# Performance work log

Hardware: AMD Instinct MI355X
Metric: run time of the kernel (lower is better)

Reference implementation:

```python
import jax, jax.numpy as jnp
import numpy as np

EPS = 1e-5

def layer_norm(x, g, b):
    mu = jnp.mean(x, axis=-1, keepdims=True)
    var = jnp.mean((x - mu) ** 2, axis=-1, keepdims=True)
    return (x - mu) * jax.lax.rsqrt(var + EPS) * g + b

def setup_inputs() -> dict:
    key = jax.random.key(0)
    ks = jax.random.split(key, 13)
    B, N, C, H = 2, 2048, 1024, 16
    Dff = 4 * C
    s = lambda k, shape, fan_in: jax.random.normal(k, shape, jnp.float32) * (1.0 / np.sqrt(fan_in))
    return {
        "x": jax.random.normal(ks[0], (B, N, C), jnp.float32),
        "ln1_g": jnp.ones((C,), jnp.float32),
        "ln1_b": jnp.zeros((C,), jnp.float32),
        "qkv_w": s(ks[1], (3 * C, C), C),
        "qkv_b": jnp.zeros((3 * C,), jnp.float32),
        "proj_w": s(ks[2], (C, C), C),
        "proj_b": jnp.zeros((C,), jnp.float32),
        "ln2_g": jnp.ones((C,), jnp.float32),
        "ln2_b": jnp.zeros((C,), jnp.float32),
        "fc1_w": s(ks[3], (Dff, C), C),
        "fc1_b": jnp.zeros((Dff,), jnp.float32),
        "fc2_w": s(ks[4], (C, Dff), Dff),
        "fc2_b": jnp.zeros((C,), jnp.float32),
    }

def reference(x, ln1_g, ln1_b, qkv_w, qkv_b, proj_w, proj_b, ln2_g, ln2_b, fc1_w, fc1_b, fc2_w, fc2_b):
    B, N, C = x.shape
    H = 16
    D = C // H
    # --- attention sub-block (pre-norm) ---
    h = layer_norm(x, ln1_g, ln1_b)
    qkv = h @ qkv_w.T + qkv_b                      # [B,N,3C]
    qkv = qkv.reshape(B, N, 3, H, D).transpose(2, 0, 3, 1, 4)  # [3,B,H,N,D]
    q, k, v = qkv[0], qkv[1], qkv[2]
    attn = jnp.einsum('bhnd,bhmd->bhnm', q, k) * (D ** -0.5)   # [B,H,N,N]
    attn = jax.nn.softmax(attn, axis=-1)
    o = jnp.einsum('bhnm,bhmd->bhnd', attn, v)     # [B,H,N,D]
    o = o.transpose(0, 2, 1, 3).reshape(B, N, C)
    x = x + (o @ proj_w.T + proj_b)
    # --- MLP sub-block (pre-norm) ---
    h = layer_norm(x, ln2_g, ln2_b)
    h = jax.nn.gelu(h @ fc1_w.T + fc1_b, approximate=False)
    x = x + (h @ fc2_w.T + fc2_b)
    return x
```

## Files before the change

kernel.cpp:

```cpp
#include <hip/hip_runtime.h>
#include <hip/hip_bf16.h>
#include <math.h>

typedef __bf16 bf16;
typedef __bf16 bf16x8 __attribute__((ext_vector_type(8)));
typedef __bf16 bf16x4 __attribute__((ext_vector_type(4)));
typedef float  f32x4  __attribute__((ext_vector_type(4)));
typedef float  f32x16 __attribute__((ext_vector_type(16)));
typedef int    i32x4  __attribute__((ext_vector_type(4)));

typedef __attribute__((address_space(1))) void gvoid;
typedef __attribute__((address_space(3))) void lvoid;
#define GLOAD_LDS16(gp, lp) __builtin_amdgcn_global_load_lds((gvoid*)(gp), (lvoid*)(lp), 16, 0, 0)

__global__ __launch_bounds__(256) void prep(
    const float* __restrict__ qkvw, const float* __restrict__ projw,
    const float* __restrict__ fc1w, const float* __restrict__ fc2w,
    bf16* __restrict__ qkvw_h, bf16* __restrict__ projw_h,
    bf16* __restrict__ fc1w_h, bf16* __restrict__ fc2w_h,
    const float* __restrict__ x, const float* __restrict__ g,
    const float* __restrict__ b, bf16* __restrict__ h1) {
  int blk = blockIdx.x;
  if (blk < 12288) {
    const float* in; bf16* out; int base;
    if (blk < 3072)      { in = qkvw; out = qkvw_h; base = blk; }
    else if (blk < 4096) { in = projw; out = projw_h; base = blk - 3072; }
    else if (blk < 8192) { in = fc1w; out = fc1w_h; base = blk - 4096; }
    else                 { in = fc2w; out = fc2w_h; base = blk - 8192; }
    int i = (base * 256 + threadIdx.x) * 4;
    f32x4 v = *(const f32x4*)(in + i);
    bf16x4 o;
    #pragma unroll
    for (int e = 0; e < 4; ++e) o[e] = (bf16)v[e];
    *(bf16x4*)(out + i) = o;
    return;
  }
  int w = threadIdx.x >> 6, l = threadIdx.x & 63;
  size_t row = (size_t)(blk - 12288) * 4 + w;
  const float* xr = x + row * 1024;
  float f[16];
  #pragma unroll
  for (int c = 0; c < 4; ++c) {
    f32x4 v = *(const f32x4*)(xr + c * 256 + l * 4);
    #pragma unroll
    for (int e = 0; e < 4; ++e) f[c * 4 + e] = v[e];
  }
  float s = 0.f, ss = 0.f;
  #pragma unroll
  for (int e = 0; e < 16; ++e) { s += f[e]; ss += f[e] * f[e]; }
  #pragma unroll
  for (int d = 1; d < 64; d <<= 1) { s += __shfl_xor(s, d); ss += __shfl_xor(ss, d); }
  float mean = s * (1.f / 1024.f);
  float var  = ss * (1.f / 1024.f) - mean * mean;
  float rstd = rsqrtf(var + 1e-5f);
  #pragma unroll
  for (int c = 0; c < 4; ++c) {
    f32x4 gv = *(const f32x4*)(g + c * 256 + l * 4);
    f32x4 bv = *(const f32x4*)(b + c * 256 + l * 4);
    bf16x4 ov;
    #pragma unroll
    for (int e = 0; e < 4; ++e)
      ov[e] = (bf16)((f[c * 4 + e] - mean) * rstd * gv[e] + bv[e]);
    *(bf16x4*)(h1 + row * 1024 + c * 256 + l * 4) = ov;
  }
}

__global__ __launch_bounds__(256) void ln_f32(const float* __restrict__ x,
    const float* __restrict__ g, const float* __restrict__ b, bf16* __restrict__ out) {
  int w = threadIdx.x >> 6, l = threadIdx.x & 63;
  size_t row = (size_t)blockIdx.x * 4 + w;
  const float* xr = x + row * 1024;
  float f[16];
  #pragma unroll
  for (int c = 0; c < 4; ++c) {
    f32x4 v = *(const f32x4*)(xr + c * 256 + l * 4);
    #pragma unroll
    for (int e = 0; e < 4; ++e) f[c * 4 + e] = v[e];
  }
  float s = 0.f, ss = 0.f;
  #pragma unroll
  for (int e = 0; e < 16; ++e) { s += f[e]; ss += f[e] * f[e]; }
  #pragma unroll
  for (int d = 1; d < 64; d <<= 1) { s += __shfl_xor(s, d); ss += __shfl_xor(ss, d); }
  float mean = s * (1.f / 1024.f);
  float var  = ss * (1.f / 1024.f) - mean * mean;
  float rstd = rsqrtf(var + 1e-5f);
  #pragma unroll
  for (int c = 0; c < 4; ++c) {
    f32x4 gv = *(const f32x4*)(g + c * 256 + l * 4);
    f32x4 bv = *(const f32x4*)(b + c * 256 + l * 4);
    bf16x4 ov;
    #pragma unroll
    for (int e = 0; e < 4; ++e)
      ov[e] = (bf16)((f[c * 4 + e] - mean) * rstd * gv[e] + bv[e]);
    *(bf16x4*)(out + row * 1024 + c * 256 + l * 4) = ov;
  }
}

#define SWZ(tp) ((tp) ^ ((((tp) >> 9) & 1) << 5))
#define STAGE(buf, op, half, kt_) do { \
    const char* gp_ = (const char*)((op) ? Wp : Ap); \
    int t0_ = (op) ? colBase : rowBase; \
    const int P_ = (op) ? 12 : 13; \
    _Pragma("unroll") for (int s_ = 0; s_ < 2; ++s_) { \
      int b14_ = w * 2048 + s_ * 1024; \
      int tb_ = ((b14_ >> P_) << (P_ + 1)) | ((half) << P_) | (b14_ & ((1 << P_) - 1)); \
      int tq_ = SWZ(tb_ + l * 16); \
      GLOAD_LDS16(gp_ + ((size_t)(t0_ + (tq_ >> 7)) * lda + (size_t)(kt_) * 64) * 2 + (tq_ & 127), \
                  smbase + (buf) * 65536 + (op) * 32768 + tb_); \
    } \
  } while (0)
#define LDA(buf, mi, kk) (*(const bf16x8*)(smbase + (buf) * 65536 + \
    SWZ((wm * 128 + (mi) * 16 + lr) * 128 + (kk) * 64 + lg * 16)))
#define LDB(buf, ni, kk) (*(const bf16x8*)(smbase + (buf) * 65536 + 32768 + \
    SWZ((wn * 64 + (ni) * 16 + lr) * 128 + (kk) * 64 + lg * 16)))
#define RD_A(buf, MI0) { _Pragma("unroll") for (int i_ = 0; i_ < 4; ++i_) \
    _Pragma("unroll") for (int k_ = 0; k_ < 2; ++k_) a[i_][k_] = LDA(buf, (MI0) + i_, k_); }
#define RD_B(buf, NI0) { _Pragma("unroll") for (int j_ = 0; j_ < 2; ++j_) \
    _Pragma("unroll") for (int k_ = 0; k_ < 2; ++k_) bq[j_][k_] = LDB(buf, (NI0) + j_, k_); }
#define MFMA16(MI0, NI0) do { __builtin_amdgcn_s_setprio(1); \
    _Pragma("unroll") for (int i_ = 0; i_ < 4; ++i_) \
    _Pragma("unroll") for (int j_ = 0; j_ < 2; ++j_) \
    _Pragma("unroll") for (int k_ = 0; k_ < 2; ++k_) \
      acc[(MI0) + i_][(NI0) + j_] = __builtin_amdgcn_mfma_f32_16x16x32_bf16( \
          a[i_][k_], bq[j_][k_], acc[(MI0) + i_][(NI0) + j_], 0, 0, 0); \
    __builtin_amdgcn_s_setprio(0); } while (0)
#define BARX() __builtin_amdgcn_s_barrier()
#define LGK0() asm volatile("s_waitcnt lgkmcnt(0)")
#define VM4()  asm volatile("s_waitcnt vmcnt(4)")

template<int ACT, int HASBIAS, typename TO>
__global__ __launch_bounds__(512, 2) void gemm256(const bf16* __restrict__ Ap,
    const bf16* __restrict__ Wp, const float* __restrict__ bias,
    TO* __restrict__ out, int lda, int N, int klen, int nbx, size_t outSlice) {
  __shared__ bf16 smem_[2][2][256 * 64];
  char* smbase = (char*)smem_;
  int tid = threadIdx.x, w = tid >> 6, l = tid & 63, lr = l & 15, lg = l >> 4;
  int wm = w >> 2, wn = w & 3;
  int q = gridDim.x >> 3;
  int wg = ((int)blockIdx.x & 7) * q + ((int)blockIdx.x >> 3);
  int rowBase = (wg / nbx) * 256, colBase = (wg % nbx) * 256;
  Ap += (size_t)blockIdx.y * klen;
  Wp += (size_t)blockIdx.y * klen;
  out += (size_t)blockIdx.y * outSlice;

  f32x4 acc[8][4];
  const f32x4 fz = {0.f, 0.f, 0.f, 0.f};
  #pragma unroll
  for (int i = 0; i < 8; ++i)
    #pragma unroll
    for (int j = 0; j < 4; ++j) acc[i][j] = fz;
  bf16x8 a[4][2], bq[2][2];
  int nkt = klen >> 6;

  STAGE(0, 0, 0, 0); STAGE(0, 1, 0, 0); STAGE(0, 0, 1, 0); STAGE(0, 1, 1, 0);
  STAGE(1, 1, 0, 1); STAGE(1, 0, 1, 1);
  VM4(); BARX();

  for (int t = 0; t < nkt; t += 2) {
    int t1 = t + 1;
    int t2 = t + 2 < nkt ? t + 2 : nkt - 1;
    int t3 = t + 3 < nkt ? t + 3 : nkt - 1;
    RD_A(0, 0); RD_B(0, 0);
    STAGE(1, 0, 0, t1); STAGE(1, 1, 1, t1);
    BARX(); LGK0(); MFMA16(0, 0); BARX();
    RD_A(0, 4);
    BARX(); LGK0(); MFMA16(4, 0); BARX();
    RD_B(0, 2);
    STAGE(0, 1, 0, t2);
    BARX(); LGK0(); MFMA16(4, 2); BARX();
    RD_A(0, 0);
    STAGE(0, 0, 1, t2);
    VM4();
    BARX(); LGK0(); MFMA16(0, 2); BARX();
    RD_A(1, 0); RD_B(1, 0);
    STAGE(0, 0, 0, t2); STAGE(0, 1, 1, t2);
    BARX(); LGK0(); MFMA16(0, 0); BARX();
    RD_A(1, 4);
    BARX(); LGK0(); MFMA16(4, 0); BARX();
    RD_B(1, 2);
    STAGE(1, 1, 0, t3);
    BARX(); LGK0(); MFMA16(4, 2); BARX();
    RD_A(1, 0);
    STAGE(1, 0, 1, t3);
    VM4();
    BARX(); LGK0(); MFMA16(0, 2); BARX();
  }

  #pragma unroll
  for (int ni = 0; ni < 4; ++ni) {
    int col = colBase + wn * 64 + ni * 16 + lr;
    float bv = HASBIAS ? bias[col] : 0.f;
    #pragma unroll
    for (int mi = 0; mi < 8; ++mi) {
      #pragma unroll
      for (int jj = 0; jj < 4; ++jj) {
        int row2 = rowBase + wm * 128 + mi * 16 + lg * 4 + jj;
        float v = acc[mi][ni][jj] + bv;
        if constexpr (ACT == 1) v = 0.5f * v * (1.f + erff(v * 0.70710678118f));
        out[(size_t)row2 * N + col] = (TO)v;
      }
    }
  }
}

__global__ __launch_bounds__(256) void projred_ln(const bf16* __restrict__ part,
    const float* __restrict__ x, const float* __restrict__ pb,
    const float* __restrict__ g, const float* __restrict__ bb,
    float* __restrict__ x1, bf16* __restrict__ h2) {
  int w = threadIdx.x >> 6, l = threadIdx.x & 63;
  size_t row = (size_t)blockIdx.x * 4 + w;
  size_t rb = row * 1024;
  float f[16];
  #pragma unroll
  for (int c = 0; c < 4; ++c) {
    int off = c * 256 + l * 4;
    f32x4 v = *(const f32x4*)(x + rb + off);
    v += *(const f32x4*)(pb + off);
    #pragma unroll
    for (int sl = 0; sl < 4; ++sl) {
      bf16x4 pv = *(const bf16x4*)(part + (size_t)sl * 4194304 + rb + off);
      #pragma unroll
      for (int e = 0; e < 4; ++e) v[e] += (float)pv[e];
    }
    *(f32x4*)(x1 + rb + off) = v;
    #pragma unroll
    for (int e = 0; e < 4; ++e) f[c * 4 + e] = v[e];
  }
  float s = 0.f, ss = 0.f;
  #pragma unroll
  for (int e = 0; e < 16; ++e) { s += f[e]; ss += f[e] * f[e]; }
  #pragma unroll
  for (int d = 1; d < 64; d <<= 1) { s += __shfl_xor(s, d); ss += __shfl_xor(ss, d); }
  float mean = s * (1.f / 1024.f);
  float var  = ss * (1.f / 1024.f) - mean * mean;
  float rstd = rsqrtf(var + 1e-5f);
  #pragma unroll
  for (int c = 0; c < 4; ++c) {
    int off = c * 256 + l * 4;
    f32x4 gv = *(const f32x4*)(g + off);
    f32x4 bv = *(const f32x4*)(bb + off);
    bf16x4 ov;
    #pragma unroll
    for (int e = 0; e < 4; ++e)
      ov[e] = (bf16)((f[c * 4 + e] - mean) * rstd * gv[e] + bv[e]);
    *(bf16x4*)(h2 + rb + off) = ov;
  }
}

__global__ __launch_bounds__(256) void fc2_red(const bf16* __restrict__ part,
    const float* __restrict__ x1, const float* __restrict__ bias,
    float* __restrict__ out) {
  int i = (blockIdx.x * 256 + threadIdx.x) * 4;
  f32x4 s = *(const f32x4*)(x1 + i);
  s += *(const f32x4*)(bias + (i & 1023));
  #pragma unroll
  for (int k = 0; k < 4; ++k) {
    bf16x4 pv = *(const bf16x4*)(part + (size_t)k * 4194304 + i);
    #pragma unroll
    for (int e = 0; e < 4; ++e) s[e] += (float)pv[e];
  }
  *(f32x4*)(out + i) = s;
}

template<int ACT, int HASRES, typename TO>
__global__ __launch_bounds__(256) void gemm_bt(const bf16* __restrict__ A,
    const bf16* __restrict__ W, const float* __restrict__ bias,
    const float* __restrict__ res, TO* __restrict__ out, int M, int N, int K) {
  __shared__ bf16 As[128 * 32];
  __shared__ bf16 Bs[128 * 32];
  int tid = threadIdx.x;
  int w = tid >> 6, l = tid & 63;
  int lr = l & 15, lg = l >> 4;
  int wm = w >> 1, wn = w & 1;
  int rowBase = blockIdx.y * 128;
  int colBase = blockIdx.x * 128;
  f32x4 acc[4][4];
  const f32x4 fz = {0.f, 0.f, 0.f, 0.f};
  #pragma unroll
  for (int i = 0; i < 4; ++i)
    #pragma unroll
    for (int j = 0; j < 4; ++j) acc[i][j] = fz;
  for (int kt = 0; kt < K; kt += 32) {
    __syncthreads();
    #pragma unroll
    for (int j = 0; j < 2; ++j) {
      int u = (w * 2 + j) * 64 + l;
      int r = u >> 2, cb = (u & 3) * 8;
      GLOAD_LDS16(A + (size_t)(rowBase + r) * K + kt + cb, As + (w * 2 + j) * 512);
      GLOAD_LDS16(W + (size_t)(colBase + r) * K + kt + cb, Bs + (w * 2 + j) * 512);
    }
    __syncthreads();
    bf16x8 af[4], bfr[4];
    #pragma unroll
    for (int mi = 0; mi < 4; ++mi)
      af[mi] = *(const bf16x8*)(As + (wm * 64 + mi * 16 + lr) * 32 + lg * 8);
    #pragma unroll
    for (int ni = 0; ni < 4; ++ni)
      bfr[ni] = *(const bf16x8*)(Bs + (wn * 64 + ni * 16 + lr) * 32 + lg * 8);
    #pragma unroll
    for (int mi = 0; mi < 4; ++mi)
      #pragma unroll
      for (int ni = 0; ni < 4; ++ni)
        acc[mi][ni] = __builtin_amdgcn_mfma_f32_16x16x32_bf16(af[mi], bfr[ni], acc[mi][ni], 0, 0, 0);
  }
  #pragma unroll
  for (int ni = 0; ni < 4; ++ni) {
    int col = colBase + wn * 64 + ni * 16 + lr;
    float bv = bias[col];
    #pragma unroll
    for (int mi = 0; mi < 4; ++mi) {
      #pragma unroll
      for (int jj = 0; jj < 4; ++jj) {
        int row2 = rowBase + wm * 64 + mi * 16 + lg * 4 + jj;
        float v = acc[mi][ni][jj] + bv;
        if constexpr (ACT == 1) v = 0.5f * v * (1.f + erff(v * 0.70710678118f));
        if constexpr (HASRES)   v += res[(size_t)row2 * N + col];
        out[(size_t)row2 * N + col] = (TO)v;
      }
    }
  }
}

#define MKFRAG(S, T, OUT) do { \
    int a_, b_, c_, d_; \
    asm("v_cvt_pk_bf16_f32 %0, %1, %2" : "=v"(a_) : "v"((S)[8*(T)+0]), "v"((S)[8*(T)+1])); \
    asm("v_cvt_pk_bf16_f32 %0, %1, %2" : "=v"(b_) : "v"((S)[8*(T)+4]), "v"((S)[8*(T)+5])); \
    asm("v_cvt_pk_bf16_f32 %0, %1, %2" : "=v"(c_) : "v"((S)[8*(T)+2]), "v"((S)[8*(T)+3])); \
    asm("v_cvt_pk_bf16_f32 %0, %1, %2" : "=v"(d_) : "v"((S)[8*(T)+6]), "v"((S)[8*(T)+7])); \
    asm("v_permlane32_swap_b32 %0, %1" : "+v"(a_), "+v"(b_)); \
    asm("v_permlane32_swap_b32 %0, %1" : "+v"(c_), "+v"(d_)); \
    i32x4 wv_ = {a_, c_, b_, d_}; \
    OUT = __builtin_bit_cast(bf16x8, wv_); \
  } while (0)

__global__ __launch_bounds__(256) void attn_kernel(const bf16* __restrict__ qkv,
                                                   bf16* __restrict__ o) {
  const int Nn = 2048, C3 = 3072;
  int tid = threadIdx.x, w = tid >> 6, l = tid & 63;
  int q32 = l & 31, hi = l >> 5, hi4 = hi * 4;
  int lin = blockIdx.x;
  int wg = (lin & 7) * 64 + (lin >> 3);
  int qb = wg & 15, bh = wg >> 4;
  int b = bh >> 4, h = bh & 15;
  size_t hb = (size_t)b * Nn * C3 + h * 64;
  const bf16* Qp = qkv + hb;
  __shared__ bf16 Ks[2][64 * 64];
  __shared__ bf16 Vt[2][64 * 64];

  int q0w = qb * 128 + w * 32;
  bf16x8 qf[4];
  {
    const bf16* qrow = Qp + (size_t)(q0w + q32) * C3 + 8 * hi;
    #pragma unroll
    for (int dk = 0; dk < 4; ++dk) {
      bf16x8 t = *(const bf16x8*)(qrow + 16 * dk);
      #pragma unroll
      for (int e = 0; e < 8; ++e) qf[dk][e] = (bf16)((float)t[e] * 0.18033688f);
    }
  }

  int swz = (l & 7) << 4;
  int kr0 = tid >> 3, c80 = (tid & 7) * 8;
  char* ksw = (char*)Ks + kr0 * 128 + ((c80 * 2) ^ ((kr0 & 7) << 4));
  char* vtw = (char*)Vt + w * 1024;
  int l2 = l * 2;
  const char* abase = (const char*)Ks + q32 * 128;
  const char* vbase = (const char*)Vt + q32 * 128;
  int doff[4];
  #pragma unroll
  for (int dk = 0; dk < 4; ++dk) doff[dk] = (32 * dk + 16 * hi) ^ swz;

  const bf16* kp0 = qkv + hb + 1024 + (size_t)kr0 * C3 + c80;
  const bf16* kp1 = kp0 + (size_t)32 * C3;
  const bf16* vp0 = qkv + hb + 2048 + (size_t)l * C3 + w * 8;
  const int step = 64 * C3;

  f32x16 zz;
  #pragma unroll
  for (int i = 0; i < 16; ++i) zz[i] = 0.f;
  f32x16 oa0 = zz, oa1 = zz;
  float mrow = -1e30f, srow = 0.f;

  bf16x8 kg0 = *(const bf16x8*)kp0; kp0 += step;
  bf16x8 kg1 = *(const bf16x8*)kp1; kp1 += step;
  bf16x8 vg0 = *(const bf16x8*)vp0;
  bf16x8 vg1 = *(const bf16x8*)(vp0 + 32); vp0 += step;
  *(bf16x8*)(ksw) = kg0;
  *(bf16x8*)(ksw + 4096) = kg1;
  #pragma unroll
  for (int e = 0; e < 8; ++e) {
    *(bf16*)(vtw + e * 128 + (l2 ^ (e << 4)))        = vg0[e];
    *(bf16*)(vtw + 4096 + e * 128 + (l2 ^ (e << 4))) = vg1[e];
  }
  __syncthreads();

  for (int t = 0; t < 32; ++t) {
    int bo = (t & 1) << 13;
    if (t < 31) {
      kg0 = *(const bf16x8*)kp0; kp0 += step;
      kg1 = *(const bf16x8*)kp1; kp1 += step;
      vg0 = *(const bf16x8*)vp0;
      vg1 = *(const bf16x8*)(vp0 + 32); vp0 += step;
    }

    bf16x8 ka[2][4];
    #pragma unroll
    for (int kb = 0; kb < 2; ++kb)
      #pragma unroll
      for (int dk = 0; dk < 4; ++dk)
        ka[kb][dk] = *(const bf16x8*)(abase + bo + kb * 4096 + doff[dk]);
    f32x16 sc0 = zz, sc1 = zz;
    __builtin_amdgcn_s_setprio(1);
    #pragma unroll
    for (int dk = 0; dk < 4; ++dk) {
      sc0 = __builtin_amdgcn_mfma_f32_32x32x16_bf16(ka[0][dk], qf[dk], sc0, 0, 0, 0);
      sc1 = __builtin_amdgcn_mfma_f32_32x32x16_bf16(ka[1][dk], qf[dk], sc1, 0, 0, 0);
    }
    __builtin_amdgcn_s_setprio(0);

    float mt = sc0[0];
    #pragma unroll
    for (int r = 1; r < 16; ++r) mt = fmaxf(mt, sc0[r]);
    #pragma unroll
    for (int r = 0; r < 16; ++r) mt = fmaxf(mt, sc1[r]);
    mt = fmaxf(mt, __shfl_xor(mt, 32));
    if (!__all(mt - mrow <= 8.f)) {
      float mn = fmaxf(mrow, mt);
      float al = exp2f(mrow - mn);
      mrow = mn;
      srow *= al;
      #pragma unroll
      for (int r = 0; r < 16; ++r) {
        float alr = __shfl(al, ((r & 3) + 8 * (r >> 2)) + hi4);
        oa0[r] *= alr; oa1[r] *= alr;
      }
    }
    float rs = 0.f;
    #pragma unroll
    for (int r = 0; r < 16; ++r) { sc0[r] = exp2f(sc0[r] - mrow); rs += sc0[r]; }
    #pragma unroll
    for (int r = 0; r < 16; ++r) { sc1[r] = exp2f(sc1[r] - mrow); rs += sc1[r]; }
    rs += __shfl_xor(rs, 32);
    srow += rs;

    bf16x8 pa0, pa1, pa2, pa3;
    MKFRAG(sc0, 0, pa0);
    MKFRAG(sc0, 1, pa1);
    MKFRAG(sc1, 0, pa2);
    MKFRAG(sc1, 1, pa3);
    bf16x8 vb[2][4];
    #pragma unroll
    for (int db = 0; db < 2; ++db)
      #pragma unroll
      for (int ks = 0; ks < 4; ++ks)
        vb[db][ks] = *(const bf16x8*)(vbase + bo + db * 4096 + ((32 * ks + 16 * hi) ^ swz));
    __builtin_amdgcn_s_setprio(1);
    oa0 = __builtin_amdgcn_mfma_f32_32x32x16_bf16(pa0, vb[0][0], oa0, 0, 0, 0);
    oa0 = __builtin_amdgcn_mfma_f32_32x32x16_bf16(pa1, vb[0][1], oa0, 0, 0, 0);
    oa0 = __builtin_amdgcn_mfma_f32_32x32x16_bf16(pa2, vb[0][2], oa0, 0, 0, 0);
    oa0 = __builtin_amdgcn_mfma_f32_32x32x16_bf16(pa3, vb[0][3], oa0, 0, 0, 0);
    oa1 = __builtin_amdgcn_mfma_f32_32x32x16_bf16(pa0, vb[1][0], oa1, 0, 0, 0);
    oa1 = __builtin_amdgcn_mfma_f32_32x32x16_bf16(pa1, vb[1][1], oa1, 0, 0, 0);
    oa1 = __builtin_amdgcn_mfma_f32_32x32x16_bf16(pa2, vb[1][2], oa1, 0, 0, 0);
    oa1 = __builtin_amdgcn_mfma_f32_32x32x16_bf16(pa3, vb[1][3], oa1, 0, 0, 0);
    __builtin_amdgcn_s_setprio(0);

    if (t < 31) {
      int bo2 = bo ^ 8192;
      *(bf16x8*)(ksw + bo2) = kg0;
      *(bf16x8*)(ksw + 4096 + bo2) = kg1;
      #pragma unroll
      for (int e = 0; e < 8; ++e) {
        *(bf16*)(vtw + bo2 + e * 128 + (l2 ^ (e << 4)))        = vg0[e];
        *(bf16*)(vtw + bo2 + 4096 + e * 128 + (l2 ^ (e << 4))) = vg1[e];
      }
      __syncthreads();
    }
  }

  float inv = 1.f / srow;
  bf16* ob = o + ((size_t)b * Nn + q0w + hi4) * 1024 + h * 64 + q32;
  #pragma unroll
  for (int r = 0; r < 16; ++r) {
    const int cr = (r & 3) + 8 * (r >> 2);
    float invr = __shfl(inv, cr + hi4);
    ob[(size_t)cr * 1024]      = (bf16)(oa0[r] * invr);
    ob[(size_t)cr * 1024 + 32] = (bf16)(oa1[r] * invr);
  }
}

extern "C" void kernel_launch(void* const* d_in, const int* in_sizes, int n_in,
                              void* d_out, int out_size, void* d_ws, size_t ws_size,
                              hipStream_t stream) {
  (void)in_sizes; (void)n_in; (void)out_size;
  const float* x     = (const float*)d_in[0];
  const float* ln1g  = (const float*)d_in[1];
  const float* ln1b  = (const float*)d_in[2];
  const float* qkvw  = (const float*)d_in[3];
  const float* qkvb  = (const float*)d_in[4];
  const float* projw = (const float*)d_in[5];
  const float* projb = (const float*)d_in[6];
  const float* ln2g  = (const float*)d_in[7];
  const float* ln2b  = (const float*)d_in[8];
  const float* fc1w  = (const float*)d_in[9];
  const float* fc1b  = (const float*)d_in[10];
  const float* fc2w  = (const float*)d_in[11];
  const float* fc2b  = (const float*)d_in[12];

  char* ws = (char*)d_ws;
  bf16*  qkvw_h = (bf16*)(ws);
  bf16*  projw_h= (bf16*)(ws + (6ull  << 20));
  bf16*  fc1w_h = (bf16*)(ws + (8ull  << 20));
  bf16*  fc2w_h = (bf16*)(ws + (16ull << 20));
  bf16*  h1     = (bf16*)(ws + (24ull << 20));
  bf16*  qkv    = (bf16*)(ws + (32ull << 20));
  bf16*  ov     = (bf16*)(ws + (64ull << 20));
  float* x1     = (float*)(ws + (72ull << 20));
  bf16*  parts  = (bf16*)(ws + (96ull << 20));
  bf16*  h2  = h1;
  bf16*  ffn = qkv;
  bool big = ws_size >= (160ull << 20);

  const int M = 4096;
  prep<<<dim3(12288 + 1024), 256, 0, stream>>>(qkvw, projw, fc1w, fc2w,
      qkvw_h, projw_h, fc1w_h, fc2w_h, x, ln1g, ln1b, h1);
  gemm256<0, 1, bf16><<<dim3(192), dim3(512), 0, stream>>>(
      h1, qkvw_h, qkvb, qkv, 1024, 3072, 1024, 12, 0);
  attn_kernel<<<dim3(512), 256, 0, stream>>>(qkv, ov);
  if (big) {
    gemm256<0, 0, bf16><<<dim3(64, 4), dim3(512), 0, stream>>>(
        ov, projw_h, nullptr, parts, 1024, 1024, 256, 4, 4194304ull);
    projred_ln<<<dim3(1024), 256, 0, stream>>>(parts, x, projb, ln2g, ln2b, x1, h2);
  } else {
    gemm_bt<0, 1, float><<<dim3(8, 32), 256, 0, stream>>>(
        ov, projw_h, projb, x, x1, M, 1024, 1024);
    ln_f32<<<dim3(1024), 256, 0, stream>>>(x1, ln2g, ln2b, h2);
  }
  gemm256<1, 1, bf16><<<dim3(256), dim3(512), 0, stream>>>(
      h2, fc1w_h, fc1b, ffn, 1024, 4096, 1024, 16, 0);
  if (big) {
    gemm256<0, 0, bf16><<<dim3(64, 4), dim3(512), 0, stream>>>(
        ffn, fc2w_h, nullptr, parts, 4096, 1024, 1024, 4, 4194304ull);
    fc2_red<<<dim3(4096), 256, 0, stream>>>(parts, x1, fc2b, (float*)d_out);
  } else {
    gemm_bt<0, 1, float><<<dim3(8, 32), 256, 0, stream>>>(
        ffn, fc2w_h, fc2b, x1, (float*)d_out, M, 1024, 4096);
  }
}
```

Baseline: 266.7 us.

## Replace split-K partial buffers with fp32 atomic accumulation and unroll attention loop

```diff
diff --git a/kernel.cpp b/kernel.cpp
--- a/kernel.cpp
+++ b/kernel.cpp
@@ -19,7 +19,8 @@
     bf16* __restrict__ qkvw_h, bf16* __restrict__ projw_h,
     bf16* __restrict__ fc1w_h, bf16* __restrict__ fc2w_h,
     const float* __restrict__ x, const float* __restrict__ g,
-    const float* __restrict__ b, bf16* __restrict__ h1) {
+    const float* __restrict__ b, bf16* __restrict__ h1,
+    const float* __restrict__ projb, float* __restrict__ x1, int doX1) {
   int blk = blockIdx.x;
   if (blk < 12288) {
     const float* in; bf16* out; int base;
@@ -45,6 +46,17 @@
     #pragma unroll
     for (int e = 0; e < 4; ++e) f[c * 4 + e] = v[e];
   }
+  if (doX1) {
+    #pragma unroll
+    for (int c = 0; c < 4; ++c) {
+      int off = c * 256 + l * 4;
+      f32x4 pv = *(const f32x4*)(projb + off);
+      f32x4 ov;
+      #pragma unroll
+      for (int e = 0; e < 4; ++e) ov[e] = f[c * 4 + e] + pv[e];
+      *(f32x4*)(x1 + row * 1024 + off) = ov;
+    }
+  }
   float s = 0.f, ss = 0.f;
   #pragma unroll
   for (int e = 0; e < 16; ++e) { s += f[e]; ss += f[e] * f[e]; }
@@ -94,6 +106,46 @@
     for (int e = 0; e < 4; ++e)
       ov[e] = (bf16)((f[c * 4 + e] - mean) * rstd * gv[e] + bv[e]);
     *(bf16x4*)(out + row * 1024 + c * 256 + l * 4) = ov;
+  }
+}
+
+__global__ __launch_bounds__(256) void ln2_prep(const float* __restrict__ x1,
+    const float* __restrict__ g, const float* __restrict__ bb,
+    const float* __restrict__ fc2b, bf16* __restrict__ h2,
+    float* __restrict__ outInit) {
+  int w = threadIdx.x >> 6, l = threadIdx.x & 63;
+  size_t row = (size_t)blockIdx.x * 4 + w;
+  size_t rb = row * 1024;
+  float f[16];
+  #pragma unroll
+  for (int c = 0; c < 4; ++c) {
+    f32x4 v = *(const f32x4*)(x1 + rb + c * 256 + l * 4);
+    #pragma unroll
+    for (int e = 0; e < 4; ++e) f[c * 4 + e] = v[e];
+  }
+  float s = 0.f, ss = 0.f;
+  #pragma unroll
+  for (int e = 0; e < 16; ++e) { s += f[e]; ss += f[e] * f[e]; }
+  #pragma unroll
+  for (int d = 1; d < 64; d <<= 1) { s += __shfl_xor(s, d); ss += __shfl_xor(ss, d); }
+  float mean = s * (1.f / 1024.f);
+  float var  = ss * (1.f / 1024.f) - mean * mean;
+  float rstd = rsqrtf(var + 1e-5f);
+  #pragma unroll
+  for (int c = 0; c < 4; ++c) {
+    int off = c * 256 + l * 4;
+    f32x4 gv = *(const f32x4*)(g + off);
+    f32x4 bv = *(const f32x4*)(bb + off);
+    f32x4 fb = *(const f32x4*)(fc2b + off);
+    bf16x4 ov;
+    f32x4 oi;
+    #pragma unroll
+    for (int e = 0; e < 4; ++e) {
+      ov[e] = (bf16)((f[c * 4 + e] - mean) * rstd * gv[e] + bv[e]);
+      oi[e] = f[c * 4 + e] + fb[e];
+    }
+    *(bf16x4*)(h2 + rb + off) = ov;
+    *(f32x4*)(outInit + rb + off) = oi;
   }
 }
 
@@ -129,7 +181,7 @@
 #define LGK0() asm volatile("s_waitcnt lgkmcnt(0)")
 #define VM4()  asm volatile("s_waitcnt vmcnt(4)")
 
-template<int ACT, int HASBIAS, typename TO>
+template<int ACT, int HASBIAS, int ATOMIC, typename TO>
 __global__ __launch_bounds__(512, 2) void gemm256(const bf16* __restrict__ Ap,
     const bf16* __restrict__ Wp, const float* __restrict__ bias,
     TO* __restrict__ out, int lda, int N, int klen, int nbx, size_t outSlice) {
@@ -198,69 +250,11 @@
         int row2 = rowBase + wm * 128 + mi * 16 + lg * 4 + jj;
         float v = acc[mi][ni][jj] + bv;
         if constexpr (ACT == 1) v = 0.5f * v * (1.f + erff(v * 0.70710678118f));
-        out[(size_t)row2 * N + col] = (TO)v;
+        if constexpr (ATOMIC) atomicAdd((float*)&out[(size_t)row2 * N + col], v);
+        else                  out[(size_t)row2 * N + col] = (TO)v;
       }
     }
   }
-}
-
-__global__ __launch_bounds__(256) void projred_ln(const bf16* __restrict__ part,
-    const float* __restrict__ x, const float* __restrict__ pb,
-    const float* __restrict__ g, const float* __restrict__ bb,
-    float* __restrict__ x1, bf16* __restrict__ h2) {
-  int w = threadIdx.x >> 6, l = threadIdx.x & 63;
-  size_t row = (size_t)blockIdx.x * 4 + w;
-  size_t rb = row * 1024;
-  float f[16];
-  #pragma unroll
-  for (int c = 0; c < 4; ++c) {
-    int off = c * 256 + l * 4;
-    f32x4 v = *(const f32x4*)(x + rb + off);
-    v += *(const f32x4*)(pb + off);
-    #pragma unroll
-    for (int sl = 0; sl < 4; ++sl) {
-      bf16x4 pv = *(const bf16x4*)(part + (size_t)sl * 4194304 + rb + off);
-      #pragma unroll
-      for (int e = 0; e < 4; ++e) v[e] += (float)pv[e];
-    }
-    *(f32x4*)(x1 + rb + off) = v;
-    #pragma unroll
-    for (int e = 0; e < 4; ++e) f[c * 4 + e] = v[e];
-  }
-  float s = 0.f, ss = 0.f;
-  #pragma unroll
-  for (int e = 0; e < 16; ++e) { s += f[e]; ss += f[e] * f[e]; }
-  #pragma unroll
-  for (int d = 1; d < 64; d <<= 1) { s += __shfl_xor(s, d); ss += __shfl_xor(ss, d); }
-  float mean = s * (1.f / 1024.f);
-  float var  = ss * (1.f / 1024.f) - mean * mean;
-  float rstd = rsqrtf(var + 1e-5f);
-  #pragma unroll
-  for (int c = 0; c < 4; ++c) {
-    int off = c * 256 + l * 4;
-    f32x4 gv = *(const f32x4*)(g + off);
-    f32x4 bv = *(const f32x4*)(bb + off);
-    bf16x4 ov;
-    #pragma unroll
-    for (int e = 0; e < 4; ++e)
-      ov[e] = (bf16)((f[c * 4 + e] - mean) * rstd * gv[e] + bv[e]);
-    *(bf16x4*)(h2 + rb + off) = ov;
-  }
-}
-
-__global__ __launch_bounds__(256) void fc2_red(const bf16* __restrict__ part,
-    const float* __restrict__ x1, const float* __restrict__ bias,
-    float* __restrict__ out) {
-  int i = (blockIdx.x * 256 + threadIdx.x) * 4;
-  f32x4 s = *(const f32x4*)(x1 + i);
-  s += *(const f32x4*)(bias + (i & 1023));
-  #pragma unroll
-  for (int k = 0; k < 4; ++k) {
-    bf16x4 pv = *(const bf16x4*)(part + (size_t)k * 4194304 + i);
-    #pragma unroll
-    for (int e = 0; e < 4; ++e) s[e] += (float)pv[e];
-  }
-  *(f32x4*)(out + i) = s;
 }
 
 template<int ACT, int HASRES, typename TO>
@@ -334,6 +328,70 @@
     OUT = __builtin_bit_cast(bf16x8, wv_); \
   } while (0)
 
+#define ATILE(BO, DOLOAD, DOSTAGE) do { \
+    if (DOLOAD) { \
+      kg0 = *(const bf16x8*)kp0; kp0 += step; \
+      kg1 = *(const bf16x8*)kp1; kp1 += step; \
+      vg0 = *(const bf16x8*)vp0; \
+      vg1 = *(const bf16x8*)(vp0 + 32); vp0 += step; \
+    } \
+    bf16x8 ka[2][4]; \
+    _Pragma("unroll") for (int kb = 0; kb < 2; ++kb) \
+      _Pragma("unroll") for (int dk = 0; dk < 4; ++dk) \
+        ka[kb][dk] = *(const bf16x8*)(abase + (BO) + kb * 4096 + doff[dk]); \
+    f32x16 sc0 = zz, sc1 = zz; \
+    __builtin_amdgcn_s_setprio(1); \
+    _Pragma("unroll") for (int dk = 0; dk < 4; ++dk) { \
+      sc0 = __builtin_amdgcn_mfma_f32_32x32x16_bf16(ka[0][dk], qf[dk], sc0, 0, 0, 0); \
+      sc1 = __builtin_amdgcn_mfma_f32_32x32x16_bf16(ka[1][dk], qf[dk], sc1, 0, 0, 0); \
+    } \
+    __builtin_amdgcn_s_setprio(0); \
+    float mt = sc0[0]; \
+    _Pragma("unroll") for (int r = 1; r < 16; ++r) mt = fmaxf(mt, sc0[r]); \
+    _Pragma("unroll") for (int r = 0; r < 16; ++r) mt = fmaxf(mt, sc1[r]); \
+    mt = fmaxf(mt, __shfl_xor(mt, 32)); \
+    if (!__all(mt - mrow <= 8.f)) { \
+      float mn = fmaxf(mrow, mt); \
+      float al = exp2f(mrow - mn); \
+      mrow = mn; srow *= al; \
+      _Pragma("unroll") for (int r = 0; r < 16; ++r) { \
+        float alr = __shfl(al, ((r & 3) + 8 * (r >> 2)) + hi4); \
+        oa0[r] *= alr; oa1[r] *= alr; \
+      } \
+    } \
+    float rs = 0.f; \
+    _Pragma("unroll") for (int r = 0; r < 16; ++r) { sc0[r] = exp2f(sc0[r] - mrow); rs += sc0[r]; } \
+    _Pragma("unroll") for (int r = 0; r < 16; ++r) { sc1[r] = exp2f(sc1[r] - mrow); rs += sc1[r]; } \
+    rs += __shfl_xor(rs, 32); \
+    srow += rs; \
+    bf16x8 pa0, pa1, pa2, pa3; \
+    MKFRAG(sc0, 0, pa0); MKFRAG(sc0, 1, pa1); \
+    MKFRAG(sc1, 0, pa2); MKFRAG(sc1, 1, pa3); \
+    bf16x8 vb[2][4]; \
+    _Pragma("unroll") for (int db = 0; db < 2; ++db) \
+      _Pragma("unroll") for (int ks = 0; ks < 4; ++ks) \
+        vb[db][ks] = *(const bf16x8*)(vbase + (BO) + db * 4096 + vdoff[ks]); \
+    __builtin_amdgcn_s_setprio(1); \
+    oa0 = __builtin_amdgcn_mfma_f32_32x32x16_bf16(pa0, vb[0][0], oa0, 0, 0, 0); \
+    oa0 = __builtin_amdgcn_mfma_f32_32x32x16_bf16(pa1, vb[0][1], oa0, 0, 0, 0); \
+    oa0 = __builtin_amdgcn_mfma_f32_32x32x16_bf16(pa2, vb[0][2], oa0, 0, 0, 0); \
+    oa0 = __builtin_amdgcn_mfma_f32_32x32x16_bf16(pa3, vb[0][3], oa0, 0, 0, 0); \
+    oa1 = __builtin_amdgcn_mfma_f32_32x32x16_bf16(pa0, vb[1][0], oa1, 0, 0, 0); \
+    oa1 = __builtin_amdgcn_mfma_f32_32x32x16_bf16(pa1, vb[1][1], oa1, 0, 0, 0); \
+    oa1 = __builtin_amdgcn_mfma_f32_32x32x16_bf16(pa2, vb[1][2], oa1, 0, 0, 0); \
+    oa1 = __builtin_amdgcn_mfma_f32_32x32x16_bf16(pa3, vb[1][3], oa1, 0, 0, 0); \
+    __builtin_amdgcn_s_setprio(0); \
+    if (DOSTAGE) { \
+      *(bf16x8*)(ksw + ((BO) ^ 8192)) = kg0; \
+      *(bf16x8*)(ksw + 4096 + ((BO) ^ 8192)) = kg1; \
+      _Pragma("unroll") for (int e = 0; e < 8; ++e) { \
+        *(bf16*)(vtw + ((BO) ^ 8192) + e * 128 + (l2 ^ (e << 4)))        = vg0[e]; \
+        *(bf16*)(vtw + ((BO) ^ 8192) + 4096 + e * 128 + (l2 ^ (e << 4))) = vg1[e]; \
+      } \
+      __syncthreads(); \
+    } \
+  } while (0)
+
 __global__ __launch_bounds__(256) void attn_kernel(const bf16* __restrict__ qkv,
                                                    bf16* __restrict__ o) {
   const int Nn = 2048, C3 = 3072;
@@ -367,9 +425,12 @@
   int l2 = l * 2;
   const char* abase = (const char*)Ks + q32 * 128;
   const char* vbase = (const char*)Vt + q32 * 128;
-  int doff[4];
-  #pragma unroll
-  for (int dk = 0; dk < 4; ++dk) doff[dk] = (32 * dk + 16 * hi) ^ swz;
+  int doff[4], vdoff[4];
+  #pragma unroll
+  for (int dk = 0; dk < 4; ++dk) {
+    doff[dk]  = (32 * dk + 16 * hi) ^ swz;
+    vdoff[dk] = (32 * dk + 16 * hi) ^ swz;
+  }
 
   const bf16* kp0 = qkv + hb + 1024 + (size_t)kr0 * C3 + c80;
   const bf16* kp1 = kp0 + (size_t)32 * C3;
@@ -395,88 +456,9 @@
   }
   __syncthreads();
 
-  for (int t = 0; t < 32; ++t) {
-    int bo = (t & 1) << 13;
-    if (t < 31) {
-      kg0 = *(const bf16x8*)kp0; kp0 += step;
-      kg1 = *(const bf16x8*)kp1; kp1 += step;
-      vg0 = *(const bf16x8*)vp0;
-      vg1 = *(const bf16x8*)(vp0 + 32); vp0 += step;
-    }
-
-    bf16x8 ka[2][4];
-    #pragma unroll
-    for (int kb = 0; kb < 2; ++kb)
-      #pragma unroll
-      for (int dk = 0; dk < 4; ++dk)
-        ka[kb][dk] = *(const bf16x8*)(abase + bo + kb * 4096 + doff[dk]);
-    f32x16 sc0 = zz, sc1 = zz;
-    __builtin_amdgcn_s_setprio(1);
-    #pragma unroll
-    for (int dk = 0; dk < 4; ++dk) {
-      sc0 = __builtin_amdgcn_mfma_f32_32x32x16_bf16(ka[0][dk], qf[dk], sc0, 0, 0, 0);
-      sc1 = __builtin_amdgcn_mfma_f32_32x32x16_bf16(ka[1][dk], qf[dk], sc1, 0, 0, 0);
-    }
-    __builtin_amdgcn_s_setprio(0);
-
-    float mt = sc0[0];
-    #pragma unroll
-    for (int r = 1; r < 16; ++r) mt = fmaxf(mt, sc0[r]);
-    #pragma unroll
-    for (int r = 0; r < 16; ++r) mt = fmaxf(mt, sc1[r]);
-    mt = fmaxf(mt, __shfl_xor(mt, 32));
-    if (!__all(mt - mrow <= 8.f)) {
-      float mn = fmaxf(mrow, mt);
-      float al = exp2f(mrow - mn);
-      mrow = mn;
-      srow *= al;
-      #pragma unroll
-      for (int r = 0; r < 16; ++r) {
-        float alr = __shfl(al, ((r & 3) + 8 * (r >> 2)) + hi4);
-        oa0[r] *= alr; oa1[r] *= alr;
-      }
-    }
-    float rs = 0.f;
-    #pragma unroll
-    for (int r = 0; r < 16; ++r) { sc0[r] = exp2f(sc0[r] - mrow); rs += sc0[r]; }
-    #pragma unroll
-    for (int r = 0; r < 16; ++r) { sc1[r] = exp2f(sc1[r] - mrow); rs += sc1[r]; }
-    rs += __shfl_xor(rs, 32);
-    srow += rs;
-
-    bf16x8 pa0, pa1, pa2, pa3;
-    MKFRAG(sc0, 0, pa0);
-    MKFRAG(sc0, 1, pa1);
-    MKFRAG(sc1, 0, pa2);
-    MKFRAG(sc1, 1, pa3);
-    bf16x8 vb[2][4];
-    #pragma unroll
-    for (int db = 0; db < 2; ++db)
-      #pragma unroll
-      for (int ks = 0; ks < 4; ++ks)
-        vb[db][ks] = *(const bf16x8*)(vbase + bo + db * 4096 + ((32 * ks + 16 * hi) ^ swz));
-    __builtin_amdgcn_s_setprio(1);
-    oa0 = __builtin_amdgcn_mfma_f32_32x32x16_bf16(pa0, vb[0][0], oa0, 0, 0, 0);
-    oa0 = __builtin_amdgcn_mfma_f32_32x32x16_bf16(pa1, vb[0][1], oa0, 0, 0, 0);
-    oa0 = __builtin_amdgcn_mfma_f32_32x32x16_bf16(pa2, vb[0][2], oa0, 0, 0, 0);
-    oa0 = __builtin_amdgcn_mfma_f32_32x32x16_bf16(pa3, vb[0][3], oa0, 0, 0, 0);
-    oa1 = __builtin_amdgcn_mfma_f32_32x32x16_bf16(pa0, vb[1][0], oa1, 0, 0, 0);
-    oa1 = __builtin_amdgcn_mfma_f32_32x32x16_bf16(pa1, vb[1][1], oa1, 0, 0, 0);
-    oa1 = __builtin_amdgcn_mfma_f32_32x32x16_bf16(pa2, vb[1][2], oa1, 0, 0, 0);
-    oa1 = __builtin_amdgcn_mfma_f32_32x32x16_bf16(pa3, vb[1][3], oa1, 0, 0, 0);
-    __builtin_amdgcn_s_setprio(0);
-
-    if (t < 31) {
-      int bo2 = bo ^ 8192;
-      *(bf16x8*)(ksw + bo2) = kg0;
-      *(bf16x8*)(ksw + 4096 + bo2) = kg1;
-      #pragma unroll
-      for (int e = 0; e < 8; ++e) {
-        *(bf16*)(vtw + bo2 + e * 128 + (l2 ^ (e << 4)))        = vg0[e];
-        *(bf16*)(vtw + bo2 + 4096 + e * 128 + (l2 ^ (e << 4))) = vg1[e];
-      }
-      __syncthreads();
-    }
+  for (int tt = 0; tt < 16; ++tt) {
+    ATILE(0,    true,     true);
+    ATILE(8192, tt < 15,  tt < 15);
   }
 
   float inv = 1.f / srow;
@@ -517,32 +499,30 @@
   bf16*  qkv    = (bf16*)(ws + (32ull << 20));
   bf16*  ov     = (bf16*)(ws + (64ull << 20));
   float* x1     = (float*)(ws + (72ull << 20));
-  bf16*  parts  = (bf16*)(ws + (96ull << 20));
   bf16*  h2  = h1;
   bf16*  ffn = qkv;
   bool big = ws_size >= (160ull << 20);
 
   const int M = 4096;
   prep<<<dim3(12288 + 1024), 256, 0, stream>>>(qkvw, projw, fc1w, fc2w,
-      qkvw_h, projw_h, fc1w_h, fc2w_h, x, ln1g, ln1b, h1);
-  gemm256<0, 1, bf16><<<dim3(192), dim3(512), 0, stream>>>(
+      qkvw_h, projw_h, fc1w_h, fc2w_h, x, ln1g, ln1b, h1, projb, x1, big ? 1 : 0);
+  gemm256<0, 1, 0, bf16><<<dim3(192), dim3(512), 0, stream>>>(
       h1, qkvw_h, qkvb, qkv, 1024, 3072, 1024, 12, 0);
   attn_kernel<<<dim3(512), 256, 0, stream>>>(qkv, ov);
   if (big) {
-    gemm256<0, 0, bf16><<<dim3(64, 4), dim3(512), 0, stream>>>(
-        ov, projw_h, nullptr, parts, 1024, 1024, 256, 4, 4194304ull);
-    projred_ln<<<dim3(1024), 256, 0, stream>>>(parts, x, projb, ln2g, ln2b, x1, h2);
+    gemm256<0, 0, 1, float><<<dim3(64, 4), dim3(512), 0, stream>>>(
+        ov, projw_h, nullptr, x1, 1024, 1024, 256, 4, 0);
+    ln2_prep<<<dim3(1024), 256, 0, stream>>>(x1, ln2g, ln2b, fc2b, h2, (float*)d_out);
   } else {
     gemm_bt<0, 1, float><<<dim3(8, 32), 256, 0, stream>>>(
         ov, projw_h, projb, x, x1, M, 1024, 1024);
     ln_f32<<<dim3(1024), 256, 0, stream>>>(x1, ln2g, ln2b, h2);
   }
-  gemm256<1, 1, bf16><<<dim3(256), dim3(512), 0, stream>>>(
+  gemm256<1, 1, 0, bf16><<<dim3(256), dim3(512), 0, stream>>>(
       h2, fc1w_h, fc1b, ffn, 1024, 4096, 1024, 16, 0);
   if (big) {
-    gemm256<0, 0, bf16><<<dim3(64, 4), dim3(512), 0, stream>>>(
-        ffn, fc2w_h, nullptr, parts, 4096, 1024, 1024, 4, 4194304ull);
-    fc2_red<<<dim3(4096), 256, 0, stream>>>(parts, x1, fc2b, (float*)d_out);
+    gemm256<0, 0, 1, float><<<dim3(64, 4), dim3(512), 0, stream>>>(
+        ffn, fc2w_h, nullptr, (float*)d_out, 4096, 1024, 1024, 4, 0);
   } else {
     gemm_bt<0, 1, float><<<dim3(8, 32), 256, 0, stream>>>(
         ffn, fc2w_h, fc2b, x1, (float*)d_out, M, 1024, 4096);
```

After: 331.2 us. +24.2%, slower.
